# Kernel optimization log

Measured on AMD Instinct MI355X. Metric: run time of the kernel, lower is better.

## Reference

```python
import jax, jax.numpy as jnp
import numpy as np

N = 512          # Cartesian grid size (nRead)
C = 16           # n_coils
K = 262144       # n non-uniform k-space samples (~512 spokes x 512 readouts)


def setup_inputs() -> dict:
    key = jax.random.key(0)
    ks = jax.random.split(key, 6)
    x_real = jax.random.normal(ks[0], (C, K), jnp.float32)
    x_imag = jax.random.normal(ks[1], (C, K), jnp.float32)
    csm_real = jax.random.normal(ks[2], (C, N, N), jnp.float32)
    csm_imag = jax.random.normal(ks[3], (C, N, N), jnp.float32)
    # normalized k-space coordinates in [-0.5, 0.5)
    traj = jax.random.uniform(ks[4], (K, 2), jnp.float32, -0.5, 0.5)
    # density compensation weights (positive)
    dcf = jax.random.uniform(ks[5], (K,), jnp.float32)
    return dict(x_real=x_real, x_imag=x_imag, csm_real=csm_real,
                csm_imag=csm_imag, traj=traj, dcf=dcf)


def reference(x_real, x_imag, csm_real, csm_imag, traj, dcf):
    # Adjoint gridding NUFFT with density compensation + coil-sensitivity combine.
    # 1) density-compensate the multicoil non-Cartesian samples
    x = (x_real + 1j * x_imag) * dcf                      # [C, K] complex64
    # 2) grid (scatter-add) onto the Cartesian k-space grid (nearest-cell gridding)
    t = jax.lax.stop_gradient(traj)
    idx = jnp.round((t + 0.5) * N).astype(jnp.int32) % N  # [K, 2]
    iy, ix = idx[:, 0], idx[:, 1]
    grid = jnp.zeros((C, N, N), jnp.complex64).at[:, iy, ix].add(x)
    # 3) centered inverse FFT to image space (adjoint of DFT, scaled by N^2)
    img = jnp.fft.fftshift(
        jnp.fft.ifft2(jnp.fft.ifftshift(grid, axes=(-2, -1)), axes=(-2, -1)),
        axes=(-2, -1)) * (N * N)                          # [C, N, N]
    # 4) coil combine with conjugate sensitivity maps
    csm = csm_real + 1j * csm_imag
    out = jnp.sum(jnp.conj(csm) * img, axis=0)            # [N, N] complex64
    # return real/imag stacked, with batch dim (mimics numpy2tensor add_batch_dim)
    return jnp.stack([out.real, out.imag])[None]          # [1, 2, N, N]
```

## Files before the change

kernel.cpp:

```cpp
#include <hip/hip_runtime.h>
#include <math.h>

#define N 512
#define NN (N * N)
#define C 16
#define K 262144
#define LOG2N 9

#define SK(e) ((e) + ((e) >> 4))
#define LROW 544


__global__ __launch_bounds__(256) void prep_hist_kernel(const float2* __restrict__ traj,
                                                        const float* __restrict__ dcf,
                                                        int* __restrict__ cell,
                                                        float* __restrict__ sdcf,
                                                        int* __restrict__ count) {
    int k = blockIdx.x * 256 + threadIdx.x;
    float2 t = traj[k];
    int iy = __float2int_rn((t.x + 0.5f) * (float)N) & (N - 1);
    int ix = __float2int_rn((t.y + 0.5f) * (float)N) & (N - 1);
    int cl = iy * N + ix;
    cell[k] = cl;
    float s = ((iy + ix) & 1) ? -1.0f : 1.0f;
    sdcf[k] = dcf[k] * s;
    atomicAdd(&count[cl], 1);
}

__global__ __launch_bounds__(256) void scan_reduce_kernel(const int* __restrict__ count,
                                                          int* __restrict__ bsum) {
    __shared__ int sd[256];
    int t = threadIdx.x;
    const int4* c4 = (const int4*)count;
    int4 v = c4[blockIdx.x * 256 + t];
    sd[t] = v.x + v.y + v.z + v.w;
    __syncthreads();
    for (int d = 128; d > 0; d >>= 1) {
        if (t < d) sd[t] += sd[t + d];
        __syncthreads();
    }
    if (t == 0) bsum[blockIdx.x] = sd[0];
}

__global__ __launch_bounds__(256) void scan_top_kernel(const int* __restrict__ bsum,
                                                       int* __restrict__ boffs,
                                                       int* __restrict__ offs) {
    __shared__ int sd[256];
    int t = threadIdx.x;
    int v = bsum[t];
    sd[t] = v;
    __syncthreads();
    for (int d = 1; d < 256; d <<= 1) {
        int tmp = (t >= d) ? sd[t - d] : 0;
        __syncthreads();
        sd[t] += tmp;
        __syncthreads();
    }
    boffs[t] = sd[t] - v;
    if (t == 0) offs[NN] = K;
}

__global__ __launch_bounds__(256) void scan_final_kernel(const int* __restrict__ count,
                                                         const int* __restrict__ boffs,
                                                         int* __restrict__ offs,
                                                         int* __restrict__ cursor) {
    __shared__ int sd[256];
    int t = threadIdx.x;
    int base_idx = blockIdx.x * 256 + t;
    const int4* c4 = (const int4*)count;
    int4 v = c4[base_idx];
    int s = v.x + v.y + v.z + v.w;
    sd[t] = s;
    __syncthreads();
    for (int d = 1; d < 256; d <<= 1) {
        int tmp = (t >= d) ? sd[t - d] : 0;
        __syncthreads();
        sd[t] += tmp;
        __syncthreads();
    }
    int base = boffs[blockIdx.x] + sd[t] - s;
    int4 o;
    o.x = base;
    o.y = base + v.x;
    o.z = base + v.x + v.y;
    o.w = base + v.x + v.y + v.z;
    ((int4*)offs)[base_idx] = o;
    ((int4*)cursor)[base_idx] = o;
}

__global__ __launch_bounds__(256) void payload_kernel(const float* __restrict__ xr,
                                                      const float* __restrict__ xi,
                                                      const int* __restrict__ cell,
                                                      const float* __restrict__ sdcf,
                                                      int* __restrict__ cursor,
                                                      float2* __restrict__ pay) {
    __shared__ float tR[256][17];
    __shared__ float tI[256][17];
    __shared__ int   sp[256];
    __shared__ float sw[256];
    int t = threadIdx.x;
    int k0 = blockIdx.x * 256;
#pragma unroll
    for (int c = 0; c < C; ++c) {
        tR[t][c] = xr[(size_t)c * K + k0 + t];
        tI[t][c] = xi[(size_t)c * K + k0 + t];
    }
    int cl = cell[k0 + t];
    float w = sdcf[k0 + t];
    sp[t] = atomicAdd(&cursor[cl], 1);
    sw[t] = w;
    __syncthreads();
    int sg = t >> 4, l = t & 15;
    for (int j = sg; j < 256; j += 16) {
        int pp = sp[j];
        float ww = sw[j];
        pay[(size_t)pp * 16 + l] = make_float2(tR[j][l] * ww, tI[j][l] * ww);
    }
}

__global__ __launch_bounds__(256) void build8_kernel(const int* __restrict__ offs,
                                                     const float4* __restrict__ pay4,
                                                     float2* __restrict__ grid) {
    __shared__ float4 lds[4][LROW];
    int bid = blockIdx.x;
    int h = bid & 1;
    int r = bid >> 1;
    int t = threadIdx.x;
    int w = t >> 6;
    int l = t & 63;
    int q = h * 4 + w;
    const int* ro = offs + r * N;

    int sv[8], ev[8];
#pragma unroll
    for (int it = 0; it < 8; ++it) {
        int col = l + (it << 6);
        sv[it] = ro[col];
        ev[it] = ro[col + 1];
    }
    float4 vv[8];
#pragma unroll
    for (int it = 0; it < 8; ++it) {
        vv[it] = make_float4(0.f, 0.f, 0.f, 0.f);
        if (sv[it] < ev[it]) vv[it] = pay4[(size_t)sv[it] * 8 + q];
    }
#pragma unroll
    for (int it = 0; it < 8; ++it) {
        float4 acc = vv[it];
        for (int p = sv[it] + 1; p < ev[it]; ++p) {
            float4 v2 = pay4[(size_t)p * 8 + q];
            acc.x += v2.x; acc.y += v2.y; acc.z += v2.z; acc.w += v2.w;
        }
        int col = l + (it << 6);
        int bc = (int)(__brev((unsigned)col) >> (32 - LOG2N));
        lds[w][SK(bc)] = acc;
    }
    asm volatile("s_waitcnt lgkmcnt(0)" ::: "memory");

    for (int s = 1; s <= LOG2N; ++s) {
        int half = 1 << (s - 1);
        int m = half << 1;
#pragma unroll
        for (int i = 0; i < 4; ++i) {
            int b2 = l + (i << 6);
            int j = b2 & (half - 1);
            int grp = b2 >> (s - 1);
            int p1 = grp * m + j;
            int p2 = p1 + half;
            float ang = 6.283185307179586f * (float)j / (float)m;
            float sn, cs;
            __sincosf(ang, &sn, &cs);
            float4 v = lds[w][SK(p2)];
            float4 u = lds[w][SK(p1)];
            float tr0 = cs * v.x - sn * v.y;
            float ti0 = cs * v.y + sn * v.x;
            float tr1 = cs * v.z - sn * v.w;
            float ti1 = cs * v.w + sn * v.z;
            lds[w][SK(p2)] = make_float4(u.x - tr0, u.y - ti0, u.z - tr1, u.w - ti1);
            lds[w][SK(p1)] = make_float4(u.x + tr0, u.y + ti0, u.z + tr1, u.w + ti1);
        }
        asm volatile("s_waitcnt lgkmcnt(0)" ::: "memory");
    }

    int c0 = q * 2;
    float2* g0 = grid + (size_t)c0 * NN + (size_t)r * N;
    float2* g1 = grid + (size_t)(c0 + 1) * NN + (size_t)r * N;
    for (int i = l; i < N; i += 64) {
        float4 v = lds[w][SK(i)];
        g0[i] = make_float2(v.x, v.y);
        g1[i] = make_float2(v.z, v.w);
    }
}

__global__ __launch_bounds__(256) void colfft_kernel(float2* __restrict__ grid) {
    __shared__ float4 lds[4][LROW];
    int blk = blockIdx.x;
    int c = blk >> 6;
    int cg = blk & 63;
    int t = threadIdx.x;
    int w = t >> 6;
    int l = t & 63;
    int colb = cg * 8 + w * 2;
    float2* gp = grid + (size_t)c * NN + colb;

#pragma unroll
    for (int j = 0; j < 8; ++j) {
        int row = l + (j << 6);
        float4 v = *(const float4*)(gp + (size_t)row * N);
        int br = (int)(__brev((unsigned)row) >> (32 - LOG2N));
        lds[w][SK(br)] = v;
    }
    asm volatile("s_waitcnt lgkmcnt(0)" ::: "memory");

    for (int s = 1; s <= LOG2N; ++s) {
        int half = 1 << (s - 1);
        int m = half << 1;
#pragma unroll
        for (int i = 0; i < 4; ++i) {
            int b2 = l + (i << 6);
            int j = b2 & (half - 1);
            int grp = b2 >> (s - 1);
            int p1 = grp * m + j;
            int p2 = p1 + half;
            float ang = 6.283185307179586f * (float)j / (float)m;
            float sn, cs;
            __sincosf(ang, &sn, &cs);
            float4 v = lds[w][SK(p2)];
            float4 u = lds[w][SK(p1)];
            float tr0 = cs * v.x - sn * v.y;
            float ti0 = cs * v.y + sn * v.x;
            float tr1 = cs * v.z - sn * v.w;
            float ti1 = cs * v.w + sn * v.z;
            lds[w][SK(p2)] = make_float4(u.x - tr0, u.y - ti0, u.z - tr1, u.w - ti1);
            lds[w][SK(p1)] = make_float4(u.x + tr0, u.y + ti0, u.z + tr1, u.w + ti1);
        }
        asm volatile("s_waitcnt lgkmcnt(0)" ::: "memory");
    }

#pragma unroll
    for (int j = 0; j < 8; ++j) {
        int i = l + (j << 6);
        *(float4*)(gp + (size_t)i * N) = lds[w][SK(i)];
    }
}

__global__ __launch_bounds__(256) void combine_kernel(const float* __restrict__ csr,
                                                      const float* __restrict__ csi,
                                                      const float2* __restrict__ grid,
                                                      float* __restrict__ out) {
    int pix = blockIdx.x * 256 + threadIdx.x;
    int ny = pix >> LOG2N, nx = pix & (N - 1);
    float ar = 0.f, ai = 0.f;
#pragma unroll
    for (int c = 0; c < C; ++c) {
        float2 uv = grid[(size_t)c * NN + pix];
        float a = csr[c * NN + pix];
        float b = csi[c * NN + pix];
        ar += a * uv.x + b * uv.y;
        ai += a * uv.y - b * uv.x;
    }
    float s = ((ny + nx) & 1) ? -1.f : 1.f;
    out[pix] = s * ar;
    out[NN + pix] = s * ai;
}

extern "C" void kernel_launch(void* const* d_in, const int* in_sizes, int n_in,
                              void* d_out, int out_size, void* d_ws, size_t ws_size,
                              hipStream_t stream) {
    const float* x_real   = (const float*)d_in[0];
    const float* x_imag   = (const float*)d_in[1];
    const float* csm_real = (const float*)d_in[2];
    const float* csm_imag = (const float*)d_in[3];
    const float2* traj    = (const float2*)d_in[4];
    const float* dcf      = (const float*)d_in[5];
    float* out = (float*)d_out;

    char* ws = (char*)d_ws;
    size_t o = 0;
    float* grid  = (float*)(ws + o); o += (size_t)C * NN * 2 * sizeof(float);
    int*   cell  = (int*)(ws + o);   o += (size_t)K * sizeof(int);
    float* sdcf  = (float*)(ws + o); o += (size_t)K * sizeof(float);
    int*   count = (int*)(ws + o);   o += (size_t)NN * sizeof(int);
    int*   offs  = (int*)(ws + o);   o += ((size_t)NN + 4) * sizeof(int);
    int*   cursor= (int*)(ws + o);   o += (size_t)NN * sizeof(int);
    float2* pay  = (float2*)(ws + o); o += (size_t)K * 16 * sizeof(float2);
    int*   bsum  = (int*)(ws + o);   o += 256 * sizeof(int);
    int*   boffs = (int*)(ws + o);   o += 256 * sizeof(int);

    (void)hipMemsetAsync(count, 0, (size_t)NN * sizeof(int), stream);

    prep_hist_kernel<<<K / 256, 256, 0, stream>>>(traj, dcf, cell, sdcf, count);
    scan_reduce_kernel<<<256, 256, 0, stream>>>(count, bsum);
    scan_top_kernel<<<1, 256, 0, stream>>>(bsum, boffs, offs);
    scan_final_kernel<<<256, 256, 0, stream>>>(count, boffs, offs, cursor);
    payload_kernel<<<K / 256, 256, 0, stream>>>(x_real, x_imag, cell, sdcf, cursor, pay);
    build8_kernel<<<N * 2, 256, 0, stream>>>(offs, (const float4*)pay, (float2*)grid);
    colfft_kernel<<<C * 64, 256, 0, stream>>>((float2*)grid);
    combine_kernel<<<NN / 256, 256, 0, stream>>>(csm_real, csm_imag, (float2*)grid, out);
}
```

Before: 211.4 us.

## Use radix-4 FFT stages, merge scan kernels, pack cell/weight, prefetch second sample

Replaces the nine radix-2 LDS FFT stages in the row and column FFT kernels with four radix-4 stages plus one final radix-2 stage. This cuts LDS round-trips and wait barriers per transform. It also folds the single-block scan_top kernel into the final scan kernel, which saves a launch at the cost of every block redoing the small 256-entry scan. The cell index and signed weight are packed into one float2 array, and the build kernel prefetches the second sample per cell to expose more memory-level parallelism.

```diff
diff --git a/kernel.cpp b/kernel.cpp
--- a/kernel.cpp
+++ b/kernel.cpp
@@ -10,20 +10,86 @@
 #define SK(e) ((e) + ((e) >> 4))
 #define LROW 544
 
+__device__ __forceinline__ void rad4(float4* stripe, int p0, int h,
+                                     float c1, float s1, float c2, float s2) {
+    float4 x0 = stripe[SK(p0)];
+    float4 x1 = stripe[SK(p0 + h)];
+    float4 x2 = stripe[SK(p0 + 2 * h)];
+    float4 x3 = stripe[SK(p0 + 3 * h)];
+    float4 t, e0, e1, e2, e3, u, v;
+    t.x = c1 * x1.x - s1 * x1.y;  t.y = c1 * x1.y + s1 * x1.x;
+    t.z = c1 * x1.z - s1 * x1.w;  t.w = c1 * x1.w + s1 * x1.z;
+    e0 = make_float4(x0.x + t.x, x0.y + t.y, x0.z + t.z, x0.w + t.w);
+    e1 = make_float4(x0.x - t.x, x0.y - t.y, x0.z - t.z, x0.w - t.w);
+    t.x = c1 * x3.x - s1 * x3.y;  t.y = c1 * x3.y + s1 * x3.x;
+    t.z = c1 * x3.z - s1 * x3.w;  t.w = c1 * x3.w + s1 * x3.z;
+    e2 = make_float4(x2.x + t.x, x2.y + t.y, x2.z + t.z, x2.w + t.w);
+    e3 = make_float4(x2.x - t.x, x2.y - t.y, x2.z - t.z, x2.w - t.w);
+    u.x = c2 * e2.x - s2 * e2.y;  u.y = c2 * e2.y + s2 * e2.x;
+    u.z = c2 * e2.z - s2 * e2.w;  u.w = c2 * e2.w + s2 * e2.z;
+    stripe[SK(p0)]         = make_float4(e0.x + u.x, e0.y + u.y, e0.z + u.z, e0.w + u.w);
+    stripe[SK(p0 + 2 * h)] = make_float4(e0.x - u.x, e0.y - u.y, e0.z - u.z, e0.w - u.w);
+    v.x = -s2 * e3.x - c2 * e3.y;  v.y = c2 * e3.x - s2 * e3.y;
+    v.z = -s2 * e3.z - c2 * e3.w;  v.w = c2 * e3.z - s2 * e3.w;
+    stripe[SK(p0 + h)]     = make_float4(e1.x + v.x, e1.y + v.y, e1.z + v.z, e1.w + v.w);
+    stripe[SK(p0 + 3 * h)] = make_float4(e1.x - v.x, e1.y - v.y, e1.z - v.z, e1.w - v.w);
+}
+
+__device__ __forceinline__ void fft512_wave(float4* stripe, int l) {
+#pragma unroll
+    for (int i = 0; i < 2; ++i) {
+        int g = l + (i << 6);
+        rad4(stripe, g * 4, 1, 1.f, 0.f, 1.f, 0.f);
+    }
+    asm volatile("s_waitcnt lgkmcnt(0)" ::: "memory");
+#pragma unroll
+    for (int fs = 1; fs < 4; ++fs) {
+        int h = 1 << (2 * fs);
+#pragma unroll
+        for (int i = 0; i < 2; ++i) {
+            int g = l + (i << 6);
+            int j = g & (h - 1);
+            int grp = g >> (2 * fs);
+            int p0 = (grp << (2 * fs + 2)) + j;
+            float a1 = 6.283185307179586f * (float)j / (float)(2 * h);
+            float a2 = 0.5f * a1;
+            float s1, c1, s2, c2;
+            __sincosf(a1, &s1, &c1);
+            __sincosf(a2, &s2, &c2);
+            rad4(stripe, p0, h, c1, s1, c2, s2);
+        }
+        asm volatile("s_waitcnt lgkmcnt(0)" ::: "memory");
+    }
+#pragma unroll
+    for (int i = 0; i < 4; ++i) {
+        int b2 = l + (i << 6);
+        float ang = 6.283185307179586f * (float)b2 * (1.0f / 512.0f);
+        float sn, cs;
+        __sincosf(ang, &sn, &cs);
+        float4 v = stripe[SK(b2 + 256)];
+        float4 u = stripe[SK(b2)];
+        float tr0 = cs * v.x - sn * v.y;
+        float ti0 = cs * v.y + sn * v.x;
+        float tr1 = cs * v.z - sn * v.w;
+        float ti1 = cs * v.w + sn * v.z;
+        stripe[SK(b2 + 256)] = make_float4(u.x - tr0, u.y - ti0, u.z - tr1, u.w - ti1);
+        stripe[SK(b2)]       = make_float4(u.x + tr0, u.y + ti0, u.z + tr1, u.w + ti1);
+    }
+    asm volatile("s_waitcnt lgkmcnt(0)" ::: "memory");
+}
+
 
 __global__ __launch_bounds__(256) void prep_hist_kernel(const float2* __restrict__ traj,
                                                         const float* __restrict__ dcf,
-                                                        int* __restrict__ cell,
-                                                        float* __restrict__ sdcf,
+                                                        float2* __restrict__ cw,
                                                         int* __restrict__ count) {
     int k = blockIdx.x * 256 + threadIdx.x;
     float2 t = traj[k];
     int iy = __float2int_rn((t.x + 0.5f) * (float)N) & (N - 1);
     int ix = __float2int_rn((t.y + 0.5f) * (float)N) & (N - 1);
     int cl = iy * N + ix;
-    cell[k] = cl;
     float s = ((iy + ix) & 1) ? -1.0f : 1.0f;
-    sdcf[k] = dcf[k] * s;
+    cw[k] = make_float2(__int_as_float(cl), dcf[k] * s);
     atomicAdd(&count[cl], 1);
 }
 
@@ -42,34 +108,25 @@
     if (t == 0) bsum[blockIdx.x] = sd[0];
 }
 
-__global__ __launch_bounds__(256) void scan_top_kernel(const int* __restrict__ bsum,
-                                                       int* __restrict__ boffs,
-                                                       int* __restrict__ offs) {
+__global__ __launch_bounds__(256) void scan_final2_kernel(const int* __restrict__ count,
+                                                          const int* __restrict__ bsum,
+                                                          int* __restrict__ offs,
+                                                          int* __restrict__ cursor) {
+    __shared__ int sb[256];
     __shared__ int sd[256];
     int t = threadIdx.x;
-    int v = bsum[t];
-    sd[t] = v;
+    int b = blockIdx.x;
+    int vb = bsum[t];
+    sb[t] = vb;
     __syncthreads();
     for (int d = 1; d < 256; d <<= 1) {
-        int tmp = (t >= d) ? sd[t - d] : 0;
-        __syncthreads();
-        sd[t] += tmp;
-        __syncthreads();
-    }
-    boffs[t] = sd[t] - v;
-    if (t == 0) offs[NN] = K;
-}
-
-__global__ __launch_bounds__(256) void scan_final_kernel(const int* __restrict__ count,
-                                                         const int* __restrict__ boffs,
-                                                         int* __restrict__ offs,
-                                                         int* __restrict__ cursor) {
-    __shared__ int sd[256];
-    int t = threadIdx.x;
-    int base_idx = blockIdx.x * 256 + t;
-    const int4* c4 = (const int4*)count;
-    int4 v = c4[base_idx];
-    int s = v.x + v.y + v.z + v.w;
+        int tmp = (t >= d) ? sb[t - d] : 0;
+        __syncthreads();
+        sb[t] += tmp;
+        __syncthreads();
+    }
+    int4 c4 = ((const int4*)count)[b * 256 + t];
+    int s = c4.x + c4.y + c4.z + c4.w;
     sd[t] = s;
     __syncthreads();
     for (int d = 1; d < 256; d <<= 1) {
@@ -78,20 +135,21 @@
         sd[t] += tmp;
         __syncthreads();
     }
-    int base = boffs[blockIdx.x] + sd[t] - s;
+    int bexc = sb[b] - bsum[b];
+    int base = bexc + sd[t] - s;
     int4 o;
     o.x = base;
-    o.y = base + v.x;
-    o.z = base + v.x + v.y;
-    o.w = base + v.x + v.y + v.z;
-    ((int4*)offs)[base_idx] = o;
-    ((int4*)cursor)[base_idx] = o;
+    o.y = base + c4.x;
+    o.z = base + c4.x + c4.y;
+    o.w = base + c4.x + c4.y + c4.z;
+    ((int4*)offs)[b * 256 + t] = o;
+    ((int4*)cursor)[b * 256 + t] = o;
+    if (b == 0 && t == 0) offs[NN] = K;
 }
 
 __global__ __launch_bounds__(256) void payload_kernel(const float* __restrict__ xr,
                                                       const float* __restrict__ xi,
-                                                      const int* __restrict__ cell,
-                                                      const float* __restrict__ sdcf,
+                                                      const float2* __restrict__ cw,
                                                       int* __restrict__ cursor,
                                                       float2* __restrict__ pay) {
     __shared__ float tR[256][17];
@@ -105,10 +163,10 @@
         tR[t][c] = xr[(size_t)c * K + k0 + t];
         tI[t][c] = xi[(size_t)c * K + k0 + t];
     }
-    int cl = cell[k0 + t];
-    float w = sdcf[k0 + t];
+    float2 cwv = cw[k0 + t];
+    int cl = __float_as_int(cwv.x);
     sp[t] = atomicAdd(&cursor[cl], 1);
-    sw[t] = w;
+    sw[t] = cwv.y;
     __syncthreads();
     int sg = t >> 4, l = t & 15;
     for (int j = sg; j < 256; j += 16) {
@@ -138,7 +196,7 @@
         sv[it] = ro[col];
         ev[it] = ro[col + 1];
     }
-    float4 vv[8];
+    float4 vv[8], vv2[8];
 #pragma unroll
     for (int it = 0; it < 8; ++it) {
         vv[it] = make_float4(0.f, 0.f, 0.f, 0.f);
@@ -146,8 +204,14 @@
     }
 #pragma unroll
     for (int it = 0; it < 8; ++it) {
-        float4 acc = vv[it];
-        for (int p = sv[it] + 1; p < ev[it]; ++p) {
+        vv2[it] = make_float4(0.f, 0.f, 0.f, 0.f);
+        if (sv[it] + 1 < ev[it]) vv2[it] = pay4[(size_t)(sv[it] + 1) * 8 + q];
+    }
+#pragma unroll
+    for (int it = 0; it < 8; ++it) {
+        float4 acc = make_float4(vv[it].x + vv2[it].x, vv[it].y + vv2[it].y,
+                                 vv[it].z + vv2[it].z, vv[it].w + vv2[it].w);
+        for (int p = sv[it] + 2; p < ev[it]; ++p) {
             float4 v2 = pay4[(size_t)p * 8 + q];
             acc.x += v2.x; acc.y += v2.y; acc.z += v2.z; acc.w += v2.w;
         }
@@ -157,30 +221,7 @@
     }
     asm volatile("s_waitcnt lgkmcnt(0)" ::: "memory");
 
-    for (int s = 1; s <= LOG2N; ++s) {
-        int half = 1 << (s - 1);
-        int m = half << 1;
-#pragma unroll
-        for (int i = 0; i < 4; ++i) {
-            int b2 = l + (i << 6);
-            int j = b2 & (half - 1);
-            int grp = b2 >> (s - 1);
-            int p1 = grp * m + j;
-            int p2 = p1 + half;
-            float ang = 6.283185307179586f * (float)j / (float)m;
-            float sn, cs;
-            __sincosf(ang, &sn, &cs);
-            float4 v = lds[w][SK(p2)];
-            float4 u = lds[w][SK(p1)];
-            float tr0 = cs * v.x - sn * v.y;
-            float ti0 = cs * v.y + sn * v.x;
-            float tr1 = cs * v.z - sn * v.w;
-            float ti1 = cs * v.w + sn * v.z;
-            lds[w][SK(p2)] = make_float4(u.x - tr0, u.y - ti0, u.z - tr1, u.w - ti1);
-            lds[w][SK(p1)] = make_float4(u.x + tr0, u.y + ti0, u.z + tr1, u.w + ti1);
-        }
-        asm volatile("s_waitcnt lgkmcnt(0)" ::: "memory");
-    }
+    fft512_wave(&lds[w][0], l);
 
     int c0 = q * 2;
     float2* g0 = grid + (size_t)c0 * NN + (size_t)r * N;
@@ -212,30 +253,7 @@
     }
     asm volatile("s_waitcnt lgkmcnt(0)" ::: "memory");
 
-    for (int s = 1; s <= LOG2N; ++s) {
-        int half = 1 << (s - 1);
-        int m = half << 1;
-#pragma unroll
-        for (int i = 0; i < 4; ++i) {
-            int b2 = l + (i << 6);
-            int j = b2 & (half - 1);
-            int grp = b2 >> (s - 1);
-            int p1 = grp * m + j;
-            int p2 = p1 + half;
-            float ang = 6.283185307179586f * (float)j / (float)m;
-            float sn, cs;
-            __sincosf(ang, &sn, &cs);
-            float4 v = lds[w][SK(p2)];
-            float4 u = lds[w][SK(p1)];
-            float tr0 = cs * v.x - sn * v.y;
-            float ti0 = cs * v.y + sn * v.x;
-            float tr1 = cs * v.z - sn * v.w;
-            float ti1 = cs * v.w + sn * v.z;
-            lds[w][SK(p2)] = make_float4(u.x - tr0, u.y - ti0, u.z - tr1, u.w - ti1);
-            lds[w][SK(p1)] = make_float4(u.x + tr0, u.y + ti0, u.z + tr1, u.w + ti1);
-        }
-        asm volatile("s_waitcnt lgkmcnt(0)" ::: "memory");
-    }
+    fft512_wave(&lds[w][0], l);
 
 #pragma unroll
     for (int j = 0; j < 8; ++j) {
@@ -278,22 +296,19 @@
     char* ws = (char*)d_ws;
     size_t o = 0;
     float* grid  = (float*)(ws + o); o += (size_t)C * NN * 2 * sizeof(float);
-    int*   cell  = (int*)(ws + o);   o += (size_t)K * sizeof(int);
-    float* sdcf  = (float*)(ws + o); o += (size_t)K * sizeof(float);
+    float2* cw   = (float2*)(ws + o); o += (size_t)K * sizeof(float2);
     int*   count = (int*)(ws + o);   o += (size_t)NN * sizeof(int);
     int*   offs  = (int*)(ws + o);   o += ((size_t)NN + 4) * sizeof(int);
     int*   cursor= (int*)(ws + o);   o += (size_t)NN * sizeof(int);
     float2* pay  = (float2*)(ws + o); o += (size_t)K * 16 * sizeof(float2);
     int*   bsum  = (int*)(ws + o);   o += 256 * sizeof(int);
-    int*   boffs = (int*)(ws + o);   o += 256 * sizeof(int);
 
     (void)hipMemsetAsync(count, 0, (size_t)NN * sizeof(int), stream);
 
-    prep_hist_kernel<<<K / 256, 256, 0, stream>>>(traj, dcf, cell, sdcf, count);
+    prep_hist_kernel<<<K / 256, 256, 0, stream>>>(traj, dcf, cw, count);
     scan_reduce_kernel<<<256, 256, 0, stream>>>(count, bsum);
-    scan_top_kernel<<<1, 256, 0, stream>>>(bsum, boffs, offs);
-    scan_final_kernel<<<256, 256, 0, stream>>>(count, boffs, offs, cursor);
-    payload_kernel<<<K / 256, 256, 0, stream>>>(x_real, x_imag, cell, sdcf, cursor, pay);
+    scan_final2_kernel<<<256, 256, 0, stream>>>(count, bsum, offs, cursor);
+    payload_kernel<<<K / 256, 256, 0, stream>>>(x_real, x_imag, cw, cursor, pay);
     build8_kernel<<<N * 2, 256, 0, stream>>>(offs, (const float4*)pay, (float2*)grid);
     colfft_kernel<<<C * 64, 256, 0, stream>>>((float2*)grid);
     combine_kernel<<<NN / 256, 256, 0, stream>>>(csm_real, csm_imag, (float2*)grid, out);
```

Result: faster. 200.0 us (-5.4%).
